# Performance work log

Hardware: AMD Instinct MI355X
Metric: run time of the kernel (lower is better)

The kernel has to match this reference:

```python
import jax, jax.numpy as jnp
import numpy as np

NQ, NT, D = 8192, 8192, 128
EC, EQ, ET = 262144, 262144, 262144


def seg_softmax(logits, seg, num):
    # numerically stable segment softmax over a 1-D logits vector
    m = jax.ops.segment_max(logits, seg, num_segments=num)
    e = jnp.exp(logits - m[seg])
    s = jax.ops.segment_sum(e, seg, num_segments=num)
    return e / s[seg]


def _linear_params(key, din, dout):
    k1, k2 = jax.random.split(key)
    scale = 1.0 / np.sqrt(din)
    W = jax.random.uniform(k1, (din, dout), minval=-scale, maxval=scale, dtype=jnp.float32)
    b = jax.random.uniform(k2, (dout,), minval=-scale, maxval=scale, dtype=jnp.float32)
    return W, b


def setup_inputs():
    key = jax.random.key(0)
    ks = jax.random.split(key, 20)
    inp = {
        'Xq': jax.random.normal(ks[0], (NQ, D), dtype=jnp.float32),
        'edge_index_q': jax.random.randint(ks[1], (2, EQ), 0, NQ),
        'Xt': jax.random.normal(ks[2], (NT, D), dtype=jnp.float32),
        'edge_index_t': jax.random.randint(ks[3], (2, ET), 0, NT),
        'norm_q': jax.random.uniform(ks[4], (NQ, 1), dtype=jnp.float32),
        'norm_t': jax.random.uniform(ks[5], (NT, 1), dtype=jnp.float32),
        'cross_src': jax.random.randint(ks[6], (EC,), 0, NQ),
        'cross_dst': jax.random.randint(ks[7], (EC,), 0, NT),
        'node_mask': jnp.ones((NQ,), dtype=bool),
        'only_run_inter': 0,
    }
    names_dims = [
        ('ac_q', D, D), ('ac_t', D, D), ('vc_q', D, D), ('vc_t', D, D),
        ('mq', 2 * D, D), ('mt', 3 * D, D),
        ('aq', 2 * D, 1), ('vq', 2 * D, D), ('at', 2 * D, 1), ('vt', 2 * D, D),
    ]
    for i, (nm, din, dout) in enumerate(names_dims):
        W, b = _linear_params(ks[8 + i], din, dout)
        inp['W_' + nm] = W
        inp['b_' + nm] = b
    return inp


def reference(Xq, edge_index_q, Xt, edge_index_t, norm_q, norm_t, cross_src, cross_dst,
              node_mask, only_run_inter,
              W_ac_q, b_ac_q, W_ac_t, b_ac_t, W_vc_q, b_vc_q, W_vc_t, b_vc_t,
              W_mq, b_mq, W_mt, b_mt,
              W_aq, b_aq, W_vq, b_vq, W_at, b_at, W_vt, b_vt):
    elu = jax.nn.elu
    nq, nt, d = Xq.shape[0], Xt.shape[0], Xq.shape[1]

    # cross-graph attention logits: per (u, v) pair, dot of transformed features
    Xq_ac = elu(Xq @ W_ac_q + b_ac_q)
    Xt_ac = elu(Xt @ W_ac_t + b_ac_t)
    att_logits = jnp.sum(Xq_ac[cross_src] * Xt_ac[cross_dst], axis=-1)  # [EC]

    # t2q: aggregate target values into query nodes (faithful to original: values gathered by u indices)
    Xt_vc = elu(Xt @ W_vc_t + b_vc_t)
    att_u = seg_softmax(att_logits, cross_src, nq)[:, None]
    Xt2q = jax.ops.segment_sum(att_u * Xt_vc[cross_src], cross_src, num_segments=nq)
    Xq_merged = jnp.concatenate([Xq, Xt2q], axis=1) @ W_mq + b_mq

    # q2t: aggregate query values into target nodes, plus global query summary Q
    Xq_vc = elu(Xq @ W_vc_q + b_vc_q)
    att_v = seg_softmax(att_logits, cross_dst, nt)[:, None]
    Xq2t = jax.ops.segment_sum(att_v * Xq_vc[cross_src], cross_dst, num_segments=nt)
    Q = jnp.broadcast_to(jnp.mean(Xq, axis=0, keepdims=True), (nt, d))
    Xt_merged = jnp.concatenate([Xt, Xq2t, Q], axis=1) @ W_mt + b_mt

    if only_run_inter:
        return Xq_merged, Xt_merged

    # intra-graph edge-wise gather -> MLP -> softmax-scatter message passing
    msg_t = jnp.concatenate([Xt_merged[edge_index_t[0]], Xt_merged[edge_index_t[1]]], axis=1)  # [ET, 2D]
    a_t = seg_softmax((msg_t @ W_at + b_at)[:, 0], edge_index_t[1], nt)[:, None]
    Xt_out = jax.ops.segment_sum(a_t * (msg_t @ W_vt + b_vt), edge_index_t[1], num_segments=nt)

    msg_q = jnp.concatenate([Xq_merged[edge_index_q[0]], Xq_merged[edge_index_q[1]]], axis=1)  # [EQ, 2D]
    a_q = seg_softmax((msg_q @ W_aq + b_aq)[:, 0], edge_index_q[1], nq)[:, None]
    Xq_out = jax.ops.segment_sum(a_q * (msg_q @ W_vq + b_vq), edge_index_q[1], num_segments=nq)

    return Xq_out, Xt_out
```

## Files before the change

### kernel.cpp

```cpp
#include <hip/hip_runtime.h>
#include <math.h>


#define NBIN 8192
#define NB   64
#define NARR 4

typedef _Float16 h2f __attribute__((ext_vector_type(2)));
typedef __attribute__((ext_vector_type(8))) short short8;
typedef __attribute__((ext_vector_type(4))) float f32x4;

__device__ __forceinline__ float elu1(float x) { return x > 0.f ? x : __expf(x) - 1.f; }

__device__ __forceinline__ unsigned short f2bf(float x) {
    unsigned u = __float_as_uint(x);
    u += 0x7FFF + ((u >> 16) & 1);
    return (unsigned short)(u >> 16);
}
__device__ __forceinline__ float bflo(unsigned u) { return __uint_as_float(u << 16); }
__device__ __forceinline__ float bfhi(unsigned u) { return __uint_as_float(u & 0xFFFF0000u); }
__device__ __forceinline__ unsigned short f2h(float x) {
    return __builtin_bit_cast(unsigned short, (_Float16)x);
}

__device__ __forceinline__ float dot8_f16(const uint4 a, const uint4 b, float d) {
#if __has_builtin(__builtin_amdgcn_fdot2)
    d = __builtin_amdgcn_fdot2(__builtin_bit_cast(h2f, a.x), __builtin_bit_cast(h2f, b.x), d, false);
    d = __builtin_amdgcn_fdot2(__builtin_bit_cast(h2f, a.y), __builtin_bit_cast(h2f, b.y), d, false);
    d = __builtin_amdgcn_fdot2(__builtin_bit_cast(h2f, a.z), __builtin_bit_cast(h2f, b.z), d, false);
    d = __builtin_amdgcn_fdot2(__builtin_bit_cast(h2f, a.w), __builtin_bit_cast(h2f, b.w), d, false);
#else
    const unsigned ua[4] = { a.x, a.y, a.z, a.w };
    const unsigned ub[4] = { b.x, b.y, b.z, b.w };
    #pragma unroll
    for (int t = 0; t < 4; ++t) {
        const h2f ha = __builtin_bit_cast(h2f, ua[t]);
        const h2f hb = __builtin_bit_cast(h2f, ub[t]);
        d = fmaf((float)ha.x, (float)hb.x, d);
        d = fmaf((float)ha.y, (float)hb.y, d);
    }
#endif
    return d;
}

__device__ void wprep_body(const float* __restrict__ S, unsigned short* __restrict__ Wf)
{
    const int lane = threadIdx.x & 63;
    const int fg = threadIdx.x >> 6;
    const int l15 = lane & 15, quad = lane >> 4;
    for (int f = fg; f < 32; f += 4) {
        const int nt = f >> 2, kc = f & 3;
        const int n = nt * 16 + l15;
        const int ks = kc * 32 + quad * 8;
        unsigned short pk[8];
        #pragma unroll
        for (int jj = 0; jj < 8; ++jj)
            pk[jj] = f2bf(S[(size_t)(ks + jj) * 128 + n]);
        uint4 v;
        v.x = (unsigned)pk[0] | ((unsigned)pk[1] << 16);
        v.y = (unsigned)pk[2] | ((unsigned)pk[3] << 16);
        v.z = (unsigned)pk[4] | ((unsigned)pk[5] << 16);
        v.w = (unsigned)pk[6] | ((unsigned)pk[7] << 16);
        *(uint4*)&Wf[((size_t)f * 64 + lane) * 8] = v;
    }
}

__device__ void hist_body(int k, int a, int* h,
                          const int* __restrict__ cs, const int* __restrict__ cd,
                          const int* __restrict__ et1, const int* __restrict__ eq1,
                          unsigned short* __restrict__ partial, int EC, int ET, int EQ)
{
    const int tid = threadIdx.x;
    const int* idxs[NARR] = { cd, et1, eq1, cs };
    const int Es[NARR] = { EC, ET, EQ, EC };
    for (int b = tid; b < NBIN; b += 256) h[b] = 0;
    __syncthreads();
    const int E = Es[a];
    const int per = (E + NB - 1) / NB;
    const int lo = k * per, hi = min(E, lo + per);
    const int* idx = idxs[a];
    for (int e = lo + tid; e < hi; e += 256) atomicAdd(&h[idx[e]], 1);
    __syncthreads();
    unsigned short* P = partial + ((size_t)a * NB + k) * NBIN;
    for (int b = tid; b < NBIN; b += 256) P[b] = (unsigned short)h[b];
}

__device__ void colsum_body(int bx, const float* __restrict__ X, float* sh,
                            float* __restrict__ Qpart)
{
    const int c = threadIdx.x & 127, half = threadIdx.x >> 7;
    float s = 0.f;
    #pragma unroll 8
    for (int j = 0; j < 64; ++j)
        s += X[(size_t)(bx * 128 + half + 2 * j) * 128 + c];
    sh[threadIdx.x] = s;
    __syncthreads();
    if (half == 0) Qpart[bx * 128 + c] = sh[c] + sh[128 + c];
}

struct WSrcs { const float* s[12]; };

__global__ __launch_bounds__(256) void prep(
    const int* cs, const int* cd, const int* et1, const int* eq1,
    unsigned short* partial, int EC, int ET, int EQ,
    WSrcs ws, unsigned short* wt, const float* Xq, float* Qpart)
{
    __shared__ __align__(16) int smem_h[NBIN];
    int b = blockIdx.x;
    if (b < NARR * NB) {
        hist_body(b % NB, b / NB, smem_h, cs, cd, et1, eq1, partial, EC, ET, EQ);
    } else if ((b -= NARR * NB) < 12) {
        wprep_body(ws.s[b], wt + (size_t)b * 16384);
    } else {
        colsum_body(b - 12, Xq, (float*)smem_h, Qpart);
    }
}

__global__ void binprefix_kernel(unsigned short* __restrict__ partial, int* __restrict__ cnt)
{
    const int bin = blockIdx.x * 256 + threadIdx.x;
    const int a = blockIdx.y;
    unsigned short* P = partial + (size_t)a * NB * NBIN;
    int s = 0;
    #pragma unroll 4
    for (int k = 0; k < NB; ++k) {
        const int p = P[(size_t)k * NBIN + bin];
        P[(size_t)k * NBIN + bin] = (unsigned short)s;
        s += p;
    }
    cnt[a * NBIN + bin] = s;
}

struct MJob {
    const float* A0; const float* A1; const int* rowmask1;
    const unsigned short* W[2][2];
    const float* bias0; const float* bias1;
    float* C0; float* C1;
    unsigned short* Cb0; unsigned short* Cb1;
    unsigned short* Ch0; unsigned short* Ch1;
    const float* gvw; float* gvo;
    int act;
};

#define GEMM_SMEM (2 * 64 * 136 * 2)

__device__ void gemm_body(const MJob& j, int bx, int by, char* smem, int tid)
{
    const int c0 = by * 64;
    const int r0 = bx * 64;
    unsigned short (*AhL)[136] = (unsigned short(*)[136])smem;
    unsigned short (*AlL)[136] = (unsigned short(*)[136])(smem + 64 * 136 * 2);
    const int wv = tid >> 6, lane = tid & 63;
    const int l15 = lane & 15, quad = lane >> 4;

    f32x4 acc[2][4] = {};

    for (int pass = 0; pass < 2; ++pass) {
        const float* A = pass ? j.A1 : j.A0;
        if (!A) break;
        {
            const int row = tid >> 2, kq = (tid & 3) * 32;
            const int gr = r0 + row;
            const bool zero = pass && j.rowmask1 && (j.rowmask1[gr] == 0);
            const float* src = A + (size_t)gr * 128 + kq;
            #pragma unroll
            for (int c = 0; c < 32; c += 4) {
                float4 v = *(const float4*)(src + c);
                if (zero) v = make_float4(0.f, 0.f, 0.f, 0.f);
                const float xv[4] = { v.x, v.y, v.z, v.w };
                unsigned short hh[4], ll[4];
                #pragma unroll
                for (int u = 0; u < 4; ++u) {
                    const unsigned short hb = f2bf(xv[u]);
                    hh[u] = hb;
                    ll[u] = f2bf(xv[u] - __uint_as_float((unsigned)hb << 16));
                }
                uint2 ph, pl;
                ph.x = (unsigned)hh[0] | ((unsigned)hh[1] << 16);
                ph.y = (unsigned)hh[2] | ((unsigned)hh[3] << 16);
                pl.x = (unsigned)ll[0] | ((unsigned)ll[1] << 16);
                pl.y = (unsigned)ll[2] | ((unsigned)ll[3] << 16);
                *(uint2*)&AhL[row][kq + c] = ph;
                *(uint2*)&AlL[row][kq + c] = pl;
            }
        }
        __syncthreads();
        #pragma unroll
        for (int kc = 0; kc < 4; ++kc) {
            const short8 ah = *(const short8*)&AhL[wv * 16 + l15][kc * 32 + quad * 8];
            const short8 al = *(const short8*)&AlL[wv * 16 + l15][kc * 32 + quad * 8];
            #pragma unroll
            for (int out = 0; out < 2; ++out) {
                const unsigned short* Wf = j.W[pass][out];
                if (!Wf) continue;
                #pragma unroll
                for (int ni = 0; ni < 4; ++ni) {
                    const short8 bh = *(const short8*)&Wf[
                        ((size_t)(((c0 >> 4) + ni) * 4 + kc) * 64 + lane) * 8];
                    acc[out][ni] = __builtin_amdgcn_mfma_f32_16x16x32_bf16(ah, bh, acc[out][ni], 0, 0, 0);
                    acc[out][ni] = __builtin_amdgcn_mfma_f32_16x16x32_bf16(al, bh, acc[out][ni], 0, 0, 0);
                }
            }
        }
        __syncthreads();
    }

    #pragma unroll
    for (int out = 0; out < 2; ++out) {
        if (!j.W[0][out] && !j.W[1][out]) continue;
        const float* bias = out ? j.bias1 : j.bias0;
        float* C = out ? j.C1 : j.C0;
        unsigned short* Cb = out ? j.Cb1 : j.Cb0;
        unsigned short* Ch = out ? j.Ch1 : j.Ch0;
        const int dogv = (j.gvw != nullptr) && (out == 0);
        float p[4] = {};
        #pragma unroll
        for (int ni = 0; ni < 4; ++ni) {
            const int col = c0 + ni * 16 + l15;
            const float bvl = bias ? bias[col] : 0.f;
            const float gw = dogv ? j.gvw[col] : 0.f;
            #pragma unroll
            for (int reg = 0; reg < 4; ++reg) {
                float o = acc[out][ni][reg] + bvl;
                if (j.act) o = elu1(o);
                const int row = r0 + wv * 16 + quad * 4 + reg;
                if (C) C[(size_t)row * 128 + col] = o;
                else if (Cb) Cb[(size_t)row * 128 + col] = f2bf(o);
                else Ch[(size_t)row * 128 + col] = f2h(o);
                p[reg] = fmaf(o, gw, p[reg]);
            }
        }
        if (dogv) {
            #pragma unroll
            for (int reg = 0; reg < 4; ++reg) {
                float v = p[reg];
                v += __shfl_xor(v, 1, 64); v += __shfl_xor(v, 2, 64);
                v += __shfl_xor(v, 4, 64); v += __shfl_xor(v, 8, 64);
                if (l15 == 0)
                    j.gvo[(c0 >> 6) * NBIN + r0 + wv * 16 + quad * 4 + reg] = v;
            }
        }
    }
}

__global__ __launch_bounds__(256) void gemm_mfma(
    MJob j0, MJob j1, int ngx,
    const float* p0, const float* p1, float* o0, float* o1)
{
    __shared__ __align__(16) char smem[GEMM_SMEM];
    if ((int)blockIdx.x == ngx) {
        const int g = ((blockIdx.y << 1) | blockIdx.z) * 256 + threadIdx.x;
        for (int i = g; i < NBIN; i += 1024) o0[i] = p0[i] + p0[NBIN + i];
        for (int i = g; i < NBIN; i += 1024) o1[i] = p1[i] + p1[NBIN + i];
        return;
    }
    gemm_body(blockIdx.z ? j1 : j0, blockIdx.x, blockIdx.y, smem, threadIdx.x);
}

__device__ void scatter_body(int k, int a, char* smemraw,
    const int* __restrict__ cs, const int* __restrict__ cd,
    const int* __restrict__ et0, const int* __restrict__ et1,
    const int* __restrict__ eq0, const int* __restrict__ eq1,
    const unsigned short* __restrict__ partial, const int* __restrict__ cnt,
    int* __restrict__ offs,
    int* __restrict__ ids_cd, int* __restrict__ ids_t, int* __restrict__ ids_q,
    int EC, int ET, int EQ)
{
    int* cur = (int*)smemraw;
    int* sums = cur + NBIN;
    const int tid = threadIdx.x;
    const int Es[3] = { EC, ET, EQ };
    const int* seg[3] = { cd, et1, eq1 };
    const int* pay[3] = { cs, et0, eq0 };
    int* dst[3] = { ids_cd, ids_t, ids_q };
    const int* c = cnt + (size_t)a * NBIN;
    const unsigned short* P = partial + ((size_t)a * NB + k) * NBIN;
    int* offo = offs + (size_t)a * (NBIN + 1);
    const int base = tid * 32;
    int s = 0;
    #pragma unroll 8
    for (int i = 0; i < 32; ++i) s += c[base + i];
    sums[tid] = s;
    __syncthreads();
    for (int off = 1; off < 256; off <<= 1) {
        int v = (tid >= off) ? sums[tid - off] : 0;
        __syncthreads();
        sums[tid] += v;
        __syncthreads();
    }
    int run = tid ? sums[tid - 1] : 0;
    for (int i = 0; i < 32; ++i) {
        const int bin = base + i;
        cur[bin] = run + (int)P[bin];
        if (k == 0) offo[bin] = run;
        run += c[bin];
    }
    if (k == 0 && tid == 0) offo[NBIN] = Es[a];
    __syncthreads();
    const int per = (Es[a] + NB - 1) / NB;
    const int lo = k * per, hi = min(Es[a], lo + per);
    const int* sg = seg[a]; const int* pl = pay[a]; int* dd = dst[a];
    for (int e = lo + tid; e < hi; e += 256) {
        const int pos = atomicAdd(&cur[sg[e]], 1);
        dd[pos] = pl[e];
    }
}

__device__ void mt_extra_body(char* smemraw, const float* __restrict__ Qpart,
    const float* __restrict__ Wmt, const float* __restrict__ bmt,
    float* __restrict__ outv, int M)
{
    float* red = (float*)smemraw;
    float* Qs = red + 256;
    const int tid = threadIdx.x;
    if (tid < 128) {
        float q = 0.f;
        for (int b = 0; b < 64; ++b) q += Qpart[b * 128 + tid];
        Qs[tid] = q;
    }
    __syncthreads();
    const int cc = tid & 127, h = tid >> 7;
    const float inv = 1.0f / (float)M;
    float acc = 0.f;
    #pragma unroll 4
    for (int kk = h * 64; kk < h * 64 + 64; ++kk)
        acc = fmaf(Qs[kk] * inv, Wmt[(size_t)(256 + kk) * 128 + cc], acc);
    red[tid] = acc;
    __syncthreads();
    if (h == 0) outv[cc] = bmt[cc] + red[cc] + red[128 + cc];
}

__global__ __launch_bounds__(256) void stage3(
    const int* cs, const int* cd,
    const int* et0, const int* et1, const int* eq0, const int* eq1,
    const unsigned short* partial, const int* cnt, int* offs,
    int* ids_cd, int* ids_t, int* ids_q, int EC, int ET, int EQ,
    const float* Qpart, const float* Wmt, const float* bmt, float* mte, int M)
{
    __shared__ __align__(16) char smem[NBIN * 4 + 256 * 4];
    const int b = blockIdx.x;
    if (b < 3 * NB)
        scatter_body(b % NB, b / NB, smem, cs, cd, et0, et1, eq0, eq1,
                     partial, cnt, offs, ids_cd, ids_t, ids_q, EC, ET, EQ);
    else
        mt_extra_body(smem, Qpart, Wmt, bmt, mte, M);
}

__device__ __forceinline__ void gather_chunk_bf(
    const unsigned int* __restrict__ rows, int myid, float wv, int rem,
    int half, int cl, float4& acc)
{
    const int npairs = (rem + 1) >> 1;
    int j = 0;
    for (; j + 4 <= npairs; j += 4) {
        const int e0 = 2 * j + half, e1 = e0 + 2, e2 = e0 + 4, e3 = e0 + 6;
        const int s0 = __shfl(myid, e0, 64); const float w0 = __shfl(wv, e0, 64);
        const int s1 = __shfl(myid, e1, 64); const float w1 = __shfl(wv, e1, 64);
        const int s2 = __shfl(myid, e2, 64); const float w2 = __shfl(wv, e2, 64);
        const int s3 = __shfl(myid, e3, 64); const float w3 = __shfl(wv, e3, 64);
        const uint2 v0 = *(const uint2*)(rows + (size_t)s0 * 64 + cl * 2);
        const uint2 v1 = *(const uint2*)(rows + (size_t)s1 * 64 + cl * 2);
        const uint2 v2 = *(const uint2*)(rows + (size_t)s2 * 64 + cl * 2);
        const uint2 v3 = *(const uint2*)(rows + (size_t)s3 * 64 + cl * 2);
        acc.x = fmaf(w0, bflo(v0.x), acc.x); acc.y = fmaf(w0, bfhi(v0.x), acc.y);
        acc.z = fmaf(w0, bflo(v0.y), acc.z); acc.w = fmaf(w0, bfhi(v0.y), acc.w);
        acc.x = fmaf(w1, bflo(v1.x), acc.x); acc.y = fmaf(w1, bfhi(v1.x), acc.y);
        acc.z = fmaf(w1, bflo(v1.y), acc.z); acc.w = fmaf(w1, bfhi(v1.y), acc.w);
        acc.x = fmaf(w2, bflo(v2.x), acc.x); acc.y = fmaf(w2, bfhi(v2.x), acc.y);
        acc.z = fmaf(w2, bflo(v2.y), acc.z); acc.w = fmaf(w2, bfhi(v2.y), acc.w);
        acc.x = fmaf(w3, bflo(v3.x), acc.x); acc.y = fmaf(w3, bfhi(v3.x), acc.y);
        acc.z = fmaf(w3, bflo(v3.y), acc.z); acc.w = fmaf(w3, bfhi(v3.y), acc.w);
    }
    for (; j < npairs; ++j) {
        const int e = 2 * j + half;
        const int sv = __shfl(myid, e, 64); const float we = __shfl(wv, e, 64);
        const uint2 v = *(const uint2*)(rows + (size_t)sv * 64 + cl * 2);
        acc.x = fmaf(we, bflo(v.x), acc.x); acc.y = fmaf(we, bfhi(v.x), acc.y);
        acc.z = fmaf(we, bflo(v.y), acc.z); acc.w = fmaf(we, bfhi(v.y), acc.w);
    }
}

__global__ __launch_bounds__(256) void seg_agg_intra(
    const int* ot, const int* it, const float* nlt, const unsigned int* rt,
    const float* xt, const float* ebt, float* outt,
    const int* oq, const int* iq, const float* nlq, const unsigned int* rq,
    const float* xq, const float* ebq, float* outq, int nseg)
{
    const int* offs; const int* ids; const float* nl; const unsigned int* rows;
    const float* extra; const float* eb; float* out;
    if (blockIdx.y == 0) { offs = ot; ids = it; nl = nlt; rows = rt; extra = xt; eb = ebt; out = outt; }
    else                 { offs = oq; ids = iq; nl = nlq; rows = rq; extra = xq; eb = ebq; out = outq; }
    const int wid = (int)((blockIdx.x * blockDim.x + threadIdx.x) >> 6);
    const int lane = threadIdx.x & 63;
    if (wid >= nseg) return;
    const int lo = offs[wid], hi = offs[wid + 1];
    if (lo == hi) {
        *(float2*)(out + (size_t)wid * 128 + lane * 2) = make_float2(0.f, 0.f);
        return;
    }
    const int half = lane >> 5, cl = lane & 31;
    float m = -3.4e38f, s = 0.f;
    float4 acc = make_float4(0.f, 0.f, 0.f, 0.f);
    for (int base = lo; base < hi; base += 64) {
        const int rem = min(64, hi - base);
        int myid = 0; float l = -3.4e38f;
        if (lane < rem) { myid = ids[base + lane]; l = nl[myid]; }
        float mc = l;
        #pragma unroll
        for (int t = 32; t; t >>= 1) mc = fmaxf(mc, __shfl_xor(mc, t, 64));
        const float nm = fmaxf(m, mc);
        const float alpha = __expf(m - nm);
        const float wv = (lane < rem) ? __expf(l - nm) : 0.f;
        s = s * alpha + wv;
        acc.x *= alpha; acc.y *= alpha; acc.z *= alpha; acc.w *= alpha;
        m = nm;
        gather_chunk_bf(rows, myid, wv, rem, half, cl, acc);
    }
    #pragma unroll
    for (int t = 32; t; t >>= 1) s += __shfl_xor(s, t, 64);
    acc.x += __shfl_xor(acc.x, 32, 64); acc.y += __shfl_xor(acc.y, 32, 64);
    acc.z += __shfl_xor(acc.z, 32, 64); acc.w += __shfl_xor(acc.w, 32, 64);
    if (half == 0) {
        const float inv = 1.f / s;
        const float4 xv = *(const float4*)(extra + (size_t)wid * 128 + cl * 4);
        const float4 bv = *(const float4*)(eb + cl * 4);
        float4 o;
        o.x = fmaf(acc.x, inv, xv.x + bv.x);
        o.y = fmaf(acc.y, inv, xv.y + bv.y);
        o.z = fmaf(acc.z, inv, xv.z + bv.z);
        o.w = fmaf(acc.w, inv, xv.w + bv.w);
        *(float4*)(out + (size_t)wid * 128 + cl * 4) = o;
    }
}

__global__ __launch_bounds__(256) void seg_agg_cross(
    const int* __restrict__ offs, const int* __restrict__ ids,
    const unsigned int* __restrict__ Aqh, const unsigned int* __restrict__ Ath,
    const unsigned int* __restrict__ Vqb, float* __restrict__ out, int nseg)
{
    __shared__ unsigned int atrowh[4][64];
    const int w = threadIdx.x >> 6;
    const int lane = threadIdx.x & 63;
    const int wid = blockIdx.x * 4 + w;
    if (wid >= nseg) return;
    const int lo = offs[wid], hi = offs[wid + 1];
    if (lo == hi) {
        *(float2*)(out + (size_t)wid * 128 + lane * 2) = make_float2(0.f, 0.f);
        return;
    }
    atrowh[w][lane] = Ath[(size_t)wid * 64 + lane];
    __threadfence_block();

    const int eh = lane & 31, dh = lane >> 5, cl = lane & 31;
    float m = -3.4e38f, s = 0.f;
    float4 acc = make_float4(0.f, 0.f, 0.f, 0.f);
    for (int base = lo; base < hi; base += 32) {
        const int rem = min(32, hi - base);
        int myid = 0; float d = -3.4e38f;
        if (eh < rem) {
            myid = ids[base + eh];
            const unsigned int* ar = Aqh + (size_t)myid * 64 + dh * 32;
            const unsigned int* br = &atrowh[w][dh * 32];
            d = 0.f;
            #pragma unroll
            for (int k = 0; k < 32; k += 4)
                d = dot8_f16(*(const uint4*)(ar + k), *(const uint4*)(br + k), d);
        }
        d += __shfl_xor(d, 32, 64);
        float mc = d;
        #pragma unroll
        for (int t = 16; t; t >>= 1) mc = fmaxf(mc, __shfl_xor(mc, t, 64));
        const float nm = fmaxf(m, mc);
        const float alpha = __expf(m - nm);
        const float wv = (dh == 0 && eh < rem) ? __expf(d - nm) : 0.f;
        s = s * alpha + wv;
        acc.x *= alpha; acc.y *= alpha; acc.z *= alpha; acc.w *= alpha;
        m = nm;
        gather_chunk_bf(Vqb, myid, wv, rem, dh, cl, acc);
    }
    #pragma unroll
    for (int t = 32; t; t >>= 1) s += __shfl_xor(s, t, 64);
    acc.x += __shfl_xor(acc.x, 32, 64); acc.y += __shfl_xor(acc.y, 32, 64);
    acc.z += __shfl_xor(acc.z, 32, 64); acc.w += __shfl_xor(acc.w, 32, 64);
    if (dh == 0) {
        const float inv = 1.f / s;
        float4 o;
        o.x = acc.x * inv; o.y = acc.y * inv; o.z = acc.z * inv; o.w = acc.w * inv;
        *(float4*)(out + (size_t)wid * 128 + cl * 4) = o;
    }
}

extern "C" void kernel_launch(void* const* d_in, const int* in_sizes, int n_in,
                              void* d_out, int out_size, void* d_ws, size_t ws_size,
                              hipStream_t stream)
{
    const float* Xq    = (const float*)d_in[0];
    const int*   eqidx = (const int*)d_in[1];
    const float* Xt    = (const float*)d_in[2];
    const int*   etidx = (const int*)d_in[3];
    const int*   cs    = (const int*)d_in[6];
    const int*   cd    = (const int*)d_in[7];
    const float* W_ac_q = (const float*)d_in[10]; const float* b_ac_q = (const float*)d_in[11];
    const float* W_ac_t = (const float*)d_in[12]; const float* b_ac_t = (const float*)d_in[13];
    const float* W_vc_q = (const float*)d_in[14]; const float* b_vc_q = (const float*)d_in[15];
    const float* W_vc_t = (const float*)d_in[16]; const float* b_vc_t = (const float*)d_in[17];
    const float* W_mq   = (const float*)d_in[18]; const float* b_mq   = (const float*)d_in[19];
    const float* W_mt   = (const float*)d_in[20]; const float* b_mt   = (const float*)d_in[21];
    const float* W_aq   = (const float*)d_in[22];
    const float* W_vq   = (const float*)d_in[24]; const float* b_vq   = (const float*)d_in[25];
    const float* W_at   = (const float*)d_in[26];
    const float* W_vt   = (const float*)d_in[28]; const float* b_vt   = (const float*)d_in[29];

    const int NQ = in_sizes[0] / 128;
    const int EQ = in_sizes[1] / 2;
    const int NT = in_sizes[2] / 128;
    const int ET = in_sizes[3] / 2;
    const int EC = in_sizes[6];

    const int* eq0 = eqidx;  const int* eq1 = eqidx + EQ;
    const int* et0 = etidx;  const int* et1 = etidx + ET;

    float* base = (float*)d_ws;
    size_t off = 0;
    auto alloc = [&](size_t n) { float* p = base + off; off += n; return p; };
    float* N1 = alloc((size_t)NT * 128);
    float* N2 = alloc((size_t)NQ * 128);
    float* N3 = alloc((size_t)NT * 128);
    float* N4 = alloc((size_t)NT * 128);
    unsigned int* A0h = (unsigned int*)alloc((size_t)NQ * 64);
    unsigned int* A1h = (unsigned int*)alloc((size_t)NT * 64);
    unsigned short* B0 = (unsigned short*)alloc((size_t)NQ * 64);
    unsigned short* B1 = (unsigned short*)alloc((size_t)NT * 64);
    unsigned short* B2 = (unsigned short*)alloc((size_t)NQ * 64);
    unsigned short* WT = (unsigned short*)alloc((size_t)12 * 16384 / 2);
    float* mte  = alloc(128);
    float* st0p = alloc((size_t)2 * NBIN);
    float* sq0p = alloc((size_t)2 * NBIN);
    float* st0v = alloc((size_t)NBIN);
    float* sq0v = alloc((size_t)NBIN);
    float* Qpart = alloc((size_t)64 * 128);
    int* cnt  = (int*)alloc((size_t)NARR * NBIN);
    int* offs = (int*)alloc((size_t)3 * (NBIN + 1));
    unsigned short* partial = (unsigned short*)alloc((size_t)NARR * NB * NBIN / 2);
    int* ids_cd = (int*)alloc((size_t)EC);
    int* ids_t  = (int*)alloc((size_t)ET);
    int* ids_q  = (int*)alloc((size_t)EQ);

    float* Xq_out = (float*)d_out;
    float* Xt_out = (float*)d_out + (size_t)NQ * 128;

    const int* offs_cd = offs;
    const int* offs_t  = offs + (NBIN + 1);
    const int* offs_q  = offs + 2 * (NBIN + 1);
    const int* cnt_src = cnt + 3 * NBIN;

    auto WTp = [&](int i) { return (const unsigned short*)(WT + (size_t)i * 16384); };

    WSrcs ws;
    ws.s[0] = W_ac_q; ws.s[1] = W_vc_q; ws.s[2] = W_ac_t; ws.s[3] = W_vc_t;
    ws.s[4] = W_mq;   ws.s[5] = W_mq + 16384;
    ws.s[6] = W_mt;   ws.s[7] = W_mt + 16384;
    ws.s[8] = W_vt;   ws.s[9] = W_vt + 16384;
    ws.s[10] = W_vq;  ws.s[11] = W_vq + 16384;
    prep<<<NARR * NB + 12 + NQ / 128, 256, 0, stream>>>(
        cs, cd, et1, eq1, partial, EC, ET, EQ, ws, WT, Xq, Qpart);

    binprefix_kernel<<<dim3(NBIN / 256, NARR), 256, 0, stream>>>(partial, cnt);

    const int ngx = NQ / 64;

    MJob jq{}, jt{};
    jq.A0 = Xq; jq.W[0][0] = WTp(0); jq.W[0][1] = WTp(1);
    jq.bias0 = b_ac_q; jq.bias1 = b_vc_q;
    jq.Ch0 = (unsigned short*)A0h; jq.Cb1 = B0; jq.act = 1;
    jt.A0 = Xt; jt.W[0][0] = WTp(2); jt.W[0][1] = WTp(3);
    jt.bias0 = b_ac_t; jt.bias1 = b_vc_t;
    jt.Ch0 = (unsigned short*)A1h; jt.C1 = N3; jt.act = 1;
    gemm_mfma<<<dim3(ngx, 2, 2), 256, 0, stream>>>(jq, jt, -1, nullptr, nullptr, nullptr, nullptr);

    stage3<<<3 * NB + 1, 256, 0, stream>>>(cs, cd, et0, et1, eq0, eq1,
                                           partial, cnt, offs,
                                           ids_cd, ids_t, ids_q, EC, ET, EQ,
                                           Qpart, W_mt, b_mt, mte, NQ);

    seg_agg_cross<<<(NT + 3) / 4, 256, 0, stream>>>(offs_cd, ids_cd, A0h, A1h,
                                                    (const unsigned int*)B0, N4, NT);

    MJob mq{}, mt{};
    mq.A0 = Xq; mq.W[0][0] = WTp(4);
    mq.A1 = N3; mq.W[1][0] = WTp(5); mq.rowmask1 = cnt_src;
    mq.bias0 = b_mq; mq.C0 = N2; mq.gvw = W_aq; mq.gvo = sq0p; mq.act = 0;
    mt.A0 = Xt; mt.W[0][0] = WTp(6);
    mt.A1 = N4; mt.W[1][0] = WTp(7);
    mt.bias0 = mte; mt.C0 = N1; mt.gvw = W_at; mt.gvo = st0p; mt.act = 0;
    gemm_mfma<<<dim3(ngx, 2, 2), 256, 0, stream>>>(mq, mt, -1, nullptr, nullptr, nullptr, nullptr);

    MJob ut{}, uq{};
    ut.A0 = N1; ut.W[0][0] = WTp(8); ut.W[0][1] = WTp(9);
    ut.Cb0 = B1; ut.C1 = Xt_out; ut.act = 0;
    uq.A0 = N2; uq.W[0][0] = WTp(10); uq.W[0][1] = WTp(11);
    uq.Cb0 = B2; uq.C1 = Xq_out; uq.act = 0;
    gemm_mfma<<<dim3(ngx + 1, 2, 2), 256, 0, stream>>>(ut, uq, ngx, st0p, sq0p, st0v, sq0v);

    seg_agg_intra<<<dim3((NT + 3) / 4, 2), 256, 0, stream>>>(
        offs_t, ids_t, st0v, (const unsigned int*)B1, Xt_out, b_vt, Xt_out,
        offs_q, ids_q, sq0v, (const unsigned int*)B2, Xq_out, b_vq, Xq_out, NT);
}
```

Before: 237.7 us.

## Drop bf16 hi/lo split for late GEMMs and retile to 32-row blocks

Adds a per-job split flag so only the first cross-attention GEMM keeps the two-term bf16 hi/lo decomposition of A. The merge and value GEMMs now use a single bf16 MFMA pass, halving their MFMA and LDS work. The GEMM tile also changes from 64 rows by 64 columns to 32 rows by all 128 columns, with waves split by row group and column half. Each block therefore converts A once instead of twice across column blocks. The cost is lower precision in the later GEMM outputs, which may hurt accuracy.

New measurement: 245.0 us. 3.1% more time.

```diff
diff --git a/kernel.cpp b/kernel.cpp
--- a/kernel.cpp
+++ b/kernel.cpp
@@ -139,19 +139,20 @@
     unsigned short* Cb0; unsigned short* Cb1;
     unsigned short* Ch0; unsigned short* Ch1;
     const float* gvw; float* gvo;
-    int act;
+    int act; int split;
 };
 
-#define GEMM_SMEM (2 * 64 * 136 * 2)
-
-__device__ void gemm_body(const MJob& j, int bx, int by, char* smem, int tid)
-{
-    const int c0 = by * 64;
-    const int r0 = bx * 64;
+#define GEMM_SMEM (2 * 32 * 136 * 2)
+
+__device__ void gemm_body(const MJob& j, int bx, char* smem, int tid)
+{
+    const int r0 = bx * 32;
     unsigned short (*AhL)[136] = (unsigned short(*)[136])smem;
-    unsigned short (*AlL)[136] = (unsigned short(*)[136])(smem + 64 * 136 * 2);
+    unsigned short (*AlL)[136] = (unsigned short(*)[136])(smem + 32 * 136 * 2);
     const int wv = tid >> 6, lane = tid & 63;
+    const int rg = wv >> 1, ch = wv & 1;
     const int l15 = lane & 15, quad = lane >> 4;
+    const int c0 = ch * 64;
 
     f32x4 acc[2][4] = {};
 
@@ -159,46 +160,51 @@
         const float* A = pass ? j.A1 : j.A0;
         if (!A) break;
         {
-            const int row = tid >> 2, kq = (tid & 3) * 32;
+            const int row = tid >> 3, kcol = (tid & 7) * 16;
             const int gr = r0 + row;
             const bool zero = pass && j.rowmask1 && (j.rowmask1[gr] == 0);
-            const float* src = A + (size_t)gr * 128 + kq;
+            const float* src = A + (size_t)gr * 128 + kcol;
             #pragma unroll
-            for (int c = 0; c < 32; c += 4) {
+            for (int c = 0; c < 16; c += 4) {
                 float4 v = *(const float4*)(src + c);
                 if (zero) v = make_float4(0.f, 0.f, 0.f, 0.f);
                 const float xv[4] = { v.x, v.y, v.z, v.w };
-                unsigned short hh[4], ll[4];
+                unsigned short hh[4];
                 #pragma unroll
-                for (int u = 0; u < 4; ++u) {
-                    const unsigned short hb = f2bf(xv[u]);
-                    hh[u] = hb;
-                    ll[u] = f2bf(xv[u] - __uint_as_float((unsigned)hb << 16));
-                }
-                uint2 ph, pl;
+                for (int u = 0; u < 4; ++u) hh[u] = f2bf(xv[u]);
+                uint2 ph;
                 ph.x = (unsigned)hh[0] | ((unsigned)hh[1] << 16);
                 ph.y = (unsigned)hh[2] | ((unsigned)hh[3] << 16);
-                pl.x = (unsigned)ll[0] | ((unsigned)ll[1] << 16);
-                pl.y = (unsigned)ll[2] | ((unsigned)ll[3] << 16);
-                *(uint2*)&AhL[row][kq + c] = ph;
-                *(uint2*)&AlL[row][kq + c] = pl;
+                *(uint2*)&AhL[row][kcol + c] = ph;
+                if (j.split) {
+                    unsigned short ll[4];
+                    #pragma unroll
+                    for (int u = 0; u < 4; ++u)
+                        ll[u] = f2bf(xv[u] - __uint_as_float((unsigned)hh[u] << 16));
+                    uint2 pl;
+                    pl.x = (unsigned)ll[0] | ((unsigned)ll[1] << 16);
+                    pl.y = (unsigned)ll[2] | ((unsigned)ll[3] << 16);
+                    *(uint2*)&AlL[row][kcol + c] = pl;
+                }
             }
         }
         __syncthreads();
         #pragma unroll
         for (int kc = 0; kc < 4; ++kc) {
-            const short8 ah = *(const short8*)&AhL[wv * 16 + l15][kc * 32 + quad * 8];
-            const short8 al = *(const short8*)&AlL[wv * 16 + l15][kc * 32 + quad * 8];
+            const short8 ah = *(const short8*)&AhL[rg * 16 + l15][kc * 32 + quad * 8];
+            short8 al = {};
+            if (j.split) al = *(const short8*)&AlL[rg * 16 + l15][kc * 32 + quad * 8];
             #pragma unroll
             for (int out = 0; out < 2; ++out) {
                 const unsigned short* Wf = j.W[pass][out];
                 if (!Wf) continue;
                 #pragma unroll
                 for (int ni = 0; ni < 4; ++ni) {
-                    const short8 bh = *(const short8*)&Wf[
-                        ((size_t)(((c0 >> 4) + ni) * 4 + kc) * 64 + lane) * 8];
+                    const int nt = ch * 4 + ni;
+                    const short8 bh = *(const short8*)&Wf[((size_t)(nt * 4 + kc) * 64 + lane) * 8];
                     acc[out][ni] = __builtin_amdgcn_mfma_f32_16x16x32_bf16(ah, bh, acc[out][ni], 0, 0, 0);
-                    acc[out][ni] = __builtin_amdgcn_mfma_f32_16x16x32_bf16(al, bh, acc[out][ni], 0, 0, 0);
+                    if (j.split)
+                        acc[out][ni] = __builtin_amdgcn_mfma_f32_16x16x32_bf16(al, bh, acc[out][ni], 0, 0, 0);
                 }
             }
         }
@@ -223,7 +229,7 @@
             for (int reg = 0; reg < 4; ++reg) {
                 float o = acc[out][ni][reg] + bvl;
                 if (j.act) o = elu1(o);
-                const int row = r0 + wv * 16 + quad * 4 + reg;
+                const int row = r0 + rg * 16 + quad * 4 + reg;
                 if (C) C[(size_t)row * 128 + col] = o;
                 else if (Cb) Cb[(size_t)row * 128 + col] = f2bf(o);
                 else Ch[(size_t)row * 128 + col] = f2h(o);
@@ -237,7 +243,7 @@
                 v += __shfl_xor(v, 1, 64); v += __shfl_xor(v, 2, 64);
                 v += __shfl_xor(v, 4, 64); v += __shfl_xor(v, 8, 64);
                 if (l15 == 0)
-                    j.gvo[(c0 >> 6) * NBIN + r0 + wv * 16 + quad * 4 + reg] = v;
+                    j.gvo[ch * NBIN + r0 + rg * 16 + quad * 4 + reg] = v;
             }
         }
     }
@@ -249,12 +255,12 @@
 {
     __shared__ __align__(16) char smem[GEMM_SMEM];
     if ((int)blockIdx.x == ngx) {
-        const int g = ((blockIdx.y << 1) | blockIdx.z) * 256 + threadIdx.x;
-        for (int i = g; i < NBIN; i += 1024) o0[i] = p0[i] + p0[NBIN + i];
-        for (int i = g; i < NBIN; i += 1024) o1[i] = p1[i] + p1[NBIN + i];
+        const int g = blockIdx.z * 256 + threadIdx.x;
+        for (int i = g; i < NBIN; i += 512) o0[i] = p0[i] + p0[NBIN + i];
+        for (int i = g; i < NBIN; i += 512) o1[i] = p1[i] + p1[NBIN + i];
         return;
     }
-    gemm_body(blockIdx.z ? j1 : j0, blockIdx.x, blockIdx.y, smem, threadIdx.x);
+    gemm_body(blockIdx.z ? j1 : j0, blockIdx.x, smem, threadIdx.x);
 }
 
 __device__ void scatter_body(int k, int a, char* smemraw,
@@ -567,16 +573,16 @@
 
     binprefix_kernel<<<dim3(NBIN / 256, NARR), 256, 0, stream>>>(partial, cnt);
 
-    const int ngx = NQ / 64;
+    const int ngx = NQ / 32;
 
     MJob jq{}, jt{};
     jq.A0 = Xq; jq.W[0][0] = WTp(0); jq.W[0][1] = WTp(1);
     jq.bias0 = b_ac_q; jq.bias1 = b_vc_q;
-    jq.Ch0 = (unsigned short*)A0h; jq.Cb1 = B0; jq.act = 1;
+    jq.Ch0 = (unsigned short*)A0h; jq.Cb1 = B0; jq.act = 1; jq.split = 1;
     jt.A0 = Xt; jt.W[0][0] = WTp(2); jt.W[0][1] = WTp(3);
     jt.bias0 = b_ac_t; jt.bias1 = b_vc_t;
-    jt.Ch0 = (unsigned short*)A1h; jt.C1 = N3; jt.act = 1;
-    gemm_mfma<<<dim3(ngx, 2, 2), 256, 0, stream>>>(jq, jt, -1, nullptr, nullptr, nullptr, nullptr);
+    jt.Ch0 = (unsigned short*)A1h; jt.C1 = N3; jt.act = 1; jt.split = 1;
+    gemm_mfma<<<dim3(ngx, 1, 2), 256, 0, stream>>>(jq, jt, -1, nullptr, nullptr, nullptr, nullptr);
 
     stage3<<<3 * NB + 1, 256, 0, stream>>>(cs, cd, et0, et1, eq0, eq1,
                                            partial, cnt, offs,
@@ -589,18 +595,18 @@
     MJob mq{}, mt{};
     mq.A0 = Xq; mq.W[0][0] = WTp(4);
     mq.A1 = N3; mq.W[1][0] = WTp(5); mq.rowmask1 = cnt_src;
-    mq.bias0 = b_mq; mq.C0 = N2; mq.gvw = W_aq; mq.gvo = sq0p; mq.act = 0;
+    mq.bias0 = b_mq; mq.C0 = N2; mq.gvw = W_aq; mq.gvo = sq0p; mq.act = 0; mq.split = 0;
     mt.A0 = Xt; mt.W[0][0] = WTp(6);
     mt.A1 = N4; mt.W[1][0] = WTp(7);
-    mt.bias0 = mte; mt.C0 = N1; mt.gvw = W_at; mt.gvo = st0p; mt.act = 0;
-    gemm_mfma<<<dim3(ngx, 2, 2), 256, 0, stream>>>(mq, mt, -1, nullptr, nullptr, nullptr, nullptr);
+    mt.bias0 = mte; mt.C0 = N1; mt.gvw = W_at; mt.gvo = st0p; mt.act = 0; mt.split = 0;
+    gemm_mfma<<<dim3(ngx, 1, 2), 256, 0, stream>>>(mq, mt, -1, nullptr, nullptr, nullptr, nullptr);
 
     MJob ut{}, uq{};
     ut.A0 = N1; ut.W[0][0] = WTp(8); ut.W[0][1] = WTp(9);
-    ut.Cb0 = B1; ut.C1 = Xt_out; ut.act = 0;
+    ut.Cb0 = B1; ut.C1 = Xt_out; ut.act = 0; ut.split = 0;
     uq.A0 = N2; uq.W[0][0] = WTp(10); uq.W[0][1] = WTp(11);
-    uq.Cb0 = B2; uq.C1 = Xq_out; uq.act = 0;
-    gemm_mfma<<<dim3(ngx + 1, 2, 2), 256, 0, stream>>>(ut, uq, ngx, st0p, sq0p, st0v, sq0v);
+    uq.Cb0 = B2; uq.C1 = Xq_out; uq.act = 0; uq.split = 0;
+    gemm_mfma<<<dim3(ngx + 1, 1, 2), 256, 0, stream>>>(ut, uq, ngx, st0p, sq0p, st0v, sq0v);
 
     seg_agg_intra<<<dim3((NT + 3) / 4, 2), 256, 0, stream>>>(
         offs_t, ids_t, st0v, (const unsigned int*)B1, Xt_out, b_vt, Xt_out,
```
